# Kernel tuning notes

Hardware: AMD Instinct MI355X
Metric: run time of the kernel (lower is better)

## Reference

```python
import jax, jax.numpy as jnp
import numpy as np

INS, OUTS = 768, 64
B, S = 8, 2048


def setup_inputs() -> dict:
    key = jax.random.key(0)
    ks = jax.random.split(key, 7)
    scale = 1.0 / np.sqrt(INS)
    inputs = jax.random.normal(ks[0], (B, S, INS), dtype=jnp.float32)
    Wq = jax.random.uniform(ks[1], (INS, OUTS), jnp.float32, -scale, scale)
    bq = jax.random.uniform(ks[2], (OUTS,), jnp.float32, -scale, scale)
    Wk = jax.random.uniform(ks[3], (INS, OUTS), jnp.float32, -scale, scale)
    bk = jax.random.uniform(ks[4], (OUTS,), jnp.float32, -scale, scale)
    Wv = jax.random.uniform(ks[5], (INS, OUTS), jnp.float32, -scale, scale)
    bv = jax.random.uniform(ks[6], (OUTS,), jnp.float32, -scale, scale)
    return {"inputs": inputs, "Wq": Wq, "bq": bq, "Wk": Wk, "bk": bk, "Wv": Wv, "bv": bv}


def reference(inputs, Wq, bq, Wk, bk, Wv, bv):
    # QKV projections: [B, S, ins] @ [ins, outs] -> [B, S, outs]
    q = jnp.einsum('bsi,io->bso', inputs, Wq) + bq
    k = jnp.einsum('bsi,io->bso', inputs, Wk) + bk
    v = jnp.einsum('bsi,io->bso', inputs, Wv) + bv
    dim_k = k.shape[-1]
    # scores: [B, S, S] (materialized, as in the original bmm-based impl)
    att = jnp.einsum('bqd,bkd->bqk', q, k) / jnp.sqrt(jnp.asarray(dim_k, q.dtype))
    att_soft = jax.nn.softmax(att, axis=-1)
    out = jnp.einsum('bqk,bkd->bqd', att_soft, v)
    return out
```

## Files before the change

### kernel.cpp

```cpp
#include <hip/hip_runtime.h>
#include <hip/hip_bf16.h>
#include <stdint.h>

#define INS 768
#define OUTS 64
#define BB 8
#define SS 2048
#define LDP 40

typedef __attribute__((ext_vector_type(8))) short short8;
typedef __attribute__((ext_vector_type(4))) float f32x4;

__device__ inline unsigned short f2bf(float f) {
  union { float f; uint32_t u; } v; v.f = f;
  uint32_t r = v.u + 0x7FFFu + ((v.u >> 16) & 1u);
  return (unsigned short)(r >> 16);
}

__device__ inline short8 cvt8hw(float4 a, float4 b) {
  union { __hip_bfloat162 h[4]; short8 s; } u;
  u.h[0] = __float22bfloat162_rn(make_float2(a.x, a.y));
  u.h[1] = __float22bfloat162_rn(make_float2(a.z, a.w));
  u.h[2] = __float22bfloat162_rn(make_float2(b.x, b.y));
  u.h[3] = __float22bfloat162_rn(make_float2(b.z, b.w));
  return u.s;
}

__device__ inline void gl_lds16(const void* g, void* l) {
  __builtin_amdgcn_global_load_lds(
      (const __attribute__((address_space(1))) uint32_t*)g,
      (__attribute__((address_space(3))) uint32_t*)l, 16, 0, 0);
}

__device__ inline void memfence_sched() { asm volatile("" ::: "memory"); }

#define PIPE_BARRIER(N)                                        \
  do {                                                         \
    asm volatile("s_waitcnt vmcnt(" #N ")" ::: "memory");      \
    __builtin_amdgcn_s_barrier();                              \
    __builtin_amdgcn_sched_barrier(0);                         \
  } while (0)

__global__ __launch_bounds__(256) void prep(
    const float* __restrict__ Wq, const float* __restrict__ Wk,
    const float* __restrict__ Wv, unsigned short* __restrict__ WT) {
  const int idx = blockIdx.x * 256 + threadIdx.x;
  const int m = idx / (INS * OUTS);
  const int r = idx - m * (INS * OUTS);
  const int k = r >> 6, n = r & 63;
  const float* W = (m == 0) ? Wq : (m == 1) ? Wk : Wv;
  const float s = (m == 0) ? 0.125f : 1.0f;
  WT[((size_t)m * OUTS + n) * INS + k] = f2bf(W[(size_t)k * OUTS + n] * s);
}

__global__ __launch_bounds__(256) void qkv(
    const float* __restrict__ X, const unsigned short* __restrict__ WT,
    const float* __restrict__ bq, const float* __restrict__ bk,
    const float* __restrict__ bv,
    unsigned short* __restrict__ Qg, unsigned short* __restrict__ Kg,
    unsigned short* __restrict__ Vtg) {
  __shared__ __align__(16) float Xs[4][1024];
  const int tid  = threadIdx.x;
  const int wave = tid >> 6, lane = tid & 63;
  const int quad = lane >> 4, l16 = lane & 15;
  const int chg  = wave;
  const int row0 = blockIdx.x * 32;

  const int sr = tid >> 3, ss = tid & 7;
  const char* gsrc =
      (const char*)(X + (size_t)(row0 + sr) * INS) + ((ss ^ (sr & 7)) << 4);
  char* ldsb = (char*)&Xs[0][0] + wave * 1024;

  const float* Bm[3]; float scl[3]; int col0[3];
  const unsigned short* Wt[3];
#pragma unroll
  for (int nt = 0; nt < 3; ++nt) {
    const int n0 = chg * 48 + nt * 16;
    const int mat = n0 >> 6;
    col0[nt] = n0 & 63;
    Wt[nt] = WT + ((size_t)mat * OUTS + col0[nt] + l16) * INS + quad * 8;
    if (mat == 0)      { Bm[nt] = bq; scl[nt] = 0.125f; }
    else if (mat == 1) { Bm[nt] = bk; scl[nt] = 1.0f; }
    else               { Bm[nt] = bv; scl[nt] = 1.0f; }
  }

  int off0[2], off1[2];
#pragma unroll
  for (int fr = 0; fr < 2; ++fr) {
    const int lr = fr * 16 + l16;
    off0[fr] = lr * 128 + ((((quad << 1)    ) ^ (lr & 7)) << 4);
    off1[fr] = lr * 128 + ((((quad << 1) | 1) ^ (lr & 7)) << 4);
  }

  f32x4 acc[2][3];
#pragma unroll
  for (int fr = 0; fr < 2; ++fr)
#pragma unroll
    for (int nt = 0; nt < 3; ++nt) acc[fr][nt] = (f32x4){0.f, 0.f, 0.f, 0.f};

  short8 wb[3][3];

  gl_lds16(gsrc, ldsb);
#pragma unroll
  for (int nt = 0; nt < 3; ++nt)
    wb[0][nt] = *reinterpret_cast<const short8*>(Wt[nt]);
  memfence_sched();
  gl_lds16(gsrc + 128, ldsb + 4096);
  gl_lds16(gsrc + 256, ldsb + 8192);
#pragma unroll
  for (int nt = 0; nt < 3; ++nt)
    wb[1][nt] = *reinterpret_cast<const short8*>(Wt[nt] + 32);

#pragma unroll
  for (int kc = 0; kc < 24; ++kc) {
    if (kc <= 21)      PIPE_BARRIER(4);
    else if (kc == 22) PIPE_BARRIER(3);
    else               PIPE_BARRIER(0);

    const char* xb = (const char*)&Xs[kc & 3][0];
    float4 f00 = *reinterpret_cast<const float4*>(xb + off0[0]);
    float4 f01 = *reinterpret_cast<const float4*>(xb + off1[0]);
    float4 f10 = *reinterpret_cast<const float4*>(xb + off0[1]);
    float4 f11 = *reinterpret_cast<const float4*>(xb + off1[1]);
    short8 a0 = cvt8hw(f00, f01);
    short8 a1 = cvt8hw(f10, f11);
#pragma unroll
    for (int nt = 0; nt < 3; ++nt) {
      acc[0][nt] = __builtin_amdgcn_mfma_f32_16x16x32_bf16(a0, wb[kc % 3][nt], acc[0][nt], 0, 0, 0);
      acc[1][nt] = __builtin_amdgcn_mfma_f32_16x16x32_bf16(a1, wb[kc % 3][nt], acc[1][nt], 0, 0, 0);
    }
    if (kc + 3 < 24)
      gl_lds16(gsrc + (size_t)(kc + 3) * 128, ldsb + (size_t)((kc + 3) & 3) * 4096);
    if (kc + 2 < 24) {
#pragma unroll
      for (int nt = 0; nt < 3; ++nt)
        wb[(kc + 2) % 3][nt] =
            *reinterpret_cast<const short8*>(Wt[nt] + (kc + 2) * 32);
    }
  }

#pragma unroll
  for (int fr = 0; fr < 2; ++fr) {
    const int gm0 = row0 + fr * 16 + quad * 4;
#pragma unroll
    for (int nt = 0; nt < 3; ++nt) {
      const int n = chg * 48 + nt * 16 + l16;
      const float bias = Bm[nt][col0[nt] + l16] * scl[nt];
      if (n < 128) {
        unsigned short* dstbase = (n < 64) ? Qg : Kg;
        const int nn = n & 63;
#pragma unroll
        for (int r = 0; r < 4; ++r)
          dstbase[(size_t)(gm0 + r) * OUTS + nn] = f2bf(acc[fr][nt][r] + bias);
      } else {
        const int d = n - 128;
        const int batch = gm0 >> 11, s0 = gm0 & 2047;
        ushort4 pk;
        pk.x = f2bf(acc[fr][nt][0] + bias);
        pk.y = f2bf(acc[fr][nt][1] + bias);
        pk.z = f2bf(acc[fr][nt][2] + bias);
        pk.w = f2bf(acc[fr][nt][3] + bias);
        *reinterpret_cast<ushort4*>(&Vtg[((size_t)batch * OUTS + d) * SS + s0]) = pk;
      }
    }
  }
}

__global__ __launch_bounds__(256) void attn(
    const unsigned short* __restrict__ Qg, const unsigned short* __restrict__ Kg,
    const unsigned short* __restrict__ Vtg,
    float* __restrict__ OP, float* __restrict__ LS) {
  __shared__ __align__(16) char KsB[4][4096];
  __shared__ __align__(16) char VsB[4][4096];
  __shared__ __align__(16) unsigned short Ps[4][2][16 * LDP];
  const int tid  = threadIdx.x;
  const int wave = tid >> 6, lane = tid & 63;
  const int quad = lane >> 4, l16 = lane & 15;
  const int bt  = blockIdx.x >> 6;
  const int rem = blockIdx.x & 63;
  const int qb  = rem >> 2, ksl = rem & 3;
  const int q0 = qb * 128 + wave * 32;
  const unsigned short* Qb = Qg + (size_t)bt * SS * OUTS;
  const unsigned short* Kb = Kg + (size_t)bt * SS * OUTS;
  const unsigned short* Vb = Vtg + (size_t)bt * OUTS * SS;
  const int jbeg = ksl * 512;

  const int krow = wave * 8 + (lane >> 3), ks8 = lane & 7;
  const int vrow = wave * 16 + (lane >> 2), vs4 = lane & 3;
  const int vsw  = (vrow & 3) ^ ((vrow >> 2) & 3);
  const char* ksrc = (const char*)(Kb + (size_t)(jbeg + krow) * OUTS) +
                     ((ks8 ^ (krow & 7)) << 4);
  const char* vsrc = (const char*)(Vb + (size_t)vrow * SS + jbeg) +
                     ((vs4 ^ vsw) << 4);

  short8 aq[2][2];
#pragma unroll
  for (int mh = 0; mh < 2; ++mh)
#pragma unroll
    for (int ks = 0; ks < 2; ++ks)
      aq[mh][ks] = *reinterpret_cast<const short8*>(
          Qb + (size_t)(q0 + mh * 16 + l16) * OUTS + ks * 32 + quad * 8);

  int koff[2][2];
#pragma unroll
  for (int nt2 = 0; nt2 < 2; ++nt2)
#pragma unroll
    for (int ks = 0; ks < 2; ++ks)
      koff[nt2][ks] = (nt2 * 16 + l16) * 128 +
                      ((((ks << 2) | quad) ^ (l16 & 7)) << 4);
  int voff[4];
#pragma unroll
  for (int nt = 0; nt < 4; ++nt) {
    const int dr = nt * 16 + l16;
    voff[nt] = dr * 64 + ((quad ^ ((dr & 3) ^ ((dr >> 2) & 3))) << 4);
  }

  f32x4 oacc[2][4];
#pragma unroll
  for (int mh = 0; mh < 2; ++mh)
#pragma unroll
    for (int nt = 0; nt < 4; ++nt) oacc[mh][nt] = (f32x4){0.f, 0.f, 0.f, 0.f};
  float lsum[2][4] = {{0.f,0.f,0.f,0.f},{0.f,0.f,0.f,0.f}};

  memfence_sched();
  gl_lds16(ksrc,                      &KsB[0][0] + wave * 1024);
  gl_lds16(vsrc,                      &VsB[0][0] + wave * 1024);
  gl_lds16(ksrc + (size_t)1 * 4096,   &KsB[1][0] + wave * 1024);
  gl_lds16(vsrc + (size_t)1 * 64,     &VsB[1][0] + wave * 1024);
  gl_lds16(ksrc + (size_t)2 * 4096,   &KsB[2][0] + wave * 1024);
  gl_lds16(vsrc + (size_t)2 * 64,     &VsB[2][0] + wave * 1024);

#pragma unroll
  for (int kc = 0; kc < 16; ++kc) {
    if (kc <= 13)      PIPE_BARRIER(4);
    else if (kc == 14) PIPE_BARRIER(2);
    else               PIPE_BARRIER(0);

    const char* kb8 = &KsB[kc & 3][0];
    const char* vb8 = &VsB[kc & 3][0];
    short8 bk[2][2], bv[4];
#pragma unroll
    for (int nt2 = 0; nt2 < 2; ++nt2)
#pragma unroll
      for (int ks = 0; ks < 2; ++ks)
        bk[nt2][ks] = *reinterpret_cast<const short8*>(kb8 + koff[nt2][ks]);
#pragma unroll
    for (int nt = 0; nt < 4; ++nt)
      bv[nt] = *reinterpret_cast<const short8*>(vb8 + voff[nt]);

#pragma unroll
    for (int mh = 0; mh < 2; ++mh) {
      f32x4 sc[2];
      sc[0] = (f32x4){0.f,0.f,0.f,0.f}; sc[1] = (f32x4){0.f,0.f,0.f,0.f};
#pragma unroll
      for (int ks = 0; ks < 2; ++ks)
#pragma unroll
        for (int nt2 = 0; nt2 < 2; ++nt2)
          sc[nt2] = __builtin_amdgcn_mfma_f32_16x16x32_bf16(aq[mh][ks], bk[nt2][ks], sc[nt2], 0, 0, 0);

      unsigned short* Pw = Ps[wave][mh];
#pragma unroll
      for (int nt2 = 0; nt2 < 2; ++nt2)
#pragma unroll
        for (int r = 0; r < 4; ++r) {
          float p = __expf(sc[nt2][r]);
          lsum[mh][r] += p;
          Pw[(quad * 4 + r) * LDP + nt2 * 16 + l16] = f2bf(p);
        }
      short8 ap = *reinterpret_cast<const short8*>(&Pw[l16 * LDP + quad * 8]);
#pragma unroll
      for (int nt = 0; nt < 4; ++nt)
        oacc[mh][nt] = __builtin_amdgcn_mfma_f32_16x16x32_bf16(ap, bv[nt], oacc[mh][nt], 0, 0, 0);
    }

    if (kc + 3 < 16) {
      gl_lds16(ksrc + (size_t)(kc + 3) * 4096, &KsB[(kc + 3) & 3][0] + wave * 1024);
      gl_lds16(vsrc + (size_t)(kc + 3) * 64,   &VsB[(kc + 3) & 3][0] + wave * 1024);
    }
  }

#pragma unroll
  for (int st = 1; st < 16; st <<= 1)
#pragma unroll
    for (int mh = 0; mh < 2; ++mh)
#pragma unroll
      for (int r = 0; r < 4; ++r) lsum[mh][r] += __shfl_xor(lsum[mh][r], st, 64);

  float* OPb = OP + ((size_t)ksl * BB + bt) * SS * OUTS;
#pragma unroll
  for (int mh = 0; mh < 2; ++mh)
#pragma unroll
    for (int nt = 0; nt < 4; ++nt)
#pragma unroll
      for (int r = 0; r < 4; ++r) {
        int q = q0 + mh * 16 + quad * 4 + r;
        OPb[(size_t)q * OUTS + nt * 16 + l16] = oacc[mh][nt][r];
      }
  if (l16 == 0) {
#pragma unroll
    for (int mh = 0; mh < 2; ++mh)
#pragma unroll
      for (int r = 0; r < 4; ++r)
        LS[(size_t)ksl * BB * SS + bt * SS + q0 + mh * 16 + quad * 4 + r] = lsum[mh][r];
  }
}

__global__ __launch_bounds__(256) void combine(
    const float* __restrict__ OP, const float* __restrict__ LS,
    float* __restrict__ out) {
  const size_t i4 = (size_t)blockIdx.x * 256 + threadIdx.x;
  const size_t row = (i4 * 4) >> 6;
  float4 o = make_float4(0.f, 0.f, 0.f, 0.f);
  float l = 0.f;
#pragma unroll
  for (int ks = 0; ks < 4; ++ks) {
    float4 t = reinterpret_cast<const float4*>(OP + (size_t)ks * BB * SS * OUTS)[i4];
    o.x += t.x; o.y += t.y; o.z += t.z; o.w += t.w;
    l += LS[(size_t)ks * BB * SS + row];
  }
  const float inv = 1.0f / l;
  reinterpret_cast<float4*>(out)[i4] = make_float4(o.x * inv, o.y * inv, o.z * inv, o.w * inv);
}

extern "C" void kernel_launch(void* const* d_in, const int* in_sizes, int n_in,
                              void* d_out, int out_size, void* d_ws, size_t ws_size,
                              hipStream_t stream) {
  const float* X  = (const float*)d_in[0];
  const float* Wq = (const float*)d_in[1];
  const float* bq = (const float*)d_in[2];
  const float* Wk = (const float*)d_in[3];
  const float* bk = (const float*)d_in[4];
  const float* Wv = (const float*)d_in[5];
  const float* bv = (const float*)d_in[6];
  float* out = (float*)d_out;

  char* ws = (char*)d_ws;
  unsigned short* Qg  = (unsigned short*)(ws);
  unsigned short* Kg  = (unsigned short*)(ws + (size_t)2 * 1024 * 1024);
  unsigned short* Vtg = (unsigned short*)(ws + (size_t)4 * 1024 * 1024);
  unsigned short* WT  = (unsigned short*)(ws + (size_t)6 * 1024 * 1024);
  float*          OP  = (float*)(ws + (size_t)7 * 1024 * 1024);
  float*          LS  = (float*)(ws + (size_t)23 * 1024 * 1024);

  prep<<<576, 256, 0, stream>>>(Wq, Wk, Wv, WT);
  qkv<<<512, 256, 0, stream>>>(X, WT, bq, bk, bv, Qg, Kg, Vtg);
  attn<<<512, 256, 0, stream>>>(Qg, Kg, Vtg, OP, LS);
  combine<<<1024, 256, 0, stream>>>(OP, LS, out);
}
```

Measured before the change: 138.4 us.

## Fuse prep, qkv, attn and combine into one persistent cooperative kernel

Turns the four kernels into device functions and runs them in one persistent cooperative kernel of 256 blocks. Grid-wide syncs separate the stages, and each block loops over the 512 work units of qkv and attn. The aim is to remove the launch gaps and tail drains between kernels. In exchange each CU runs only one block at a time, which lowers occupancy and latency hiding. Shared memory is also reused across loop iterations without a trailing barrier, so the early prefetch of the next unit could race with reads from the previous one. The original multi-kernel path is kept as a fallback when the stream is being captured or the cooperative launch fails.

```diff
diff --git a/kernel.cpp b/kernel.cpp
--- a/kernel.cpp
+++ b/kernel.cpp
@@ -1,6 +1,9 @@
 #include <hip/hip_runtime.h>
 #include <hip/hip_bf16.h>
+#include <hip/hip_cooperative_groups.h>
 #include <stdint.h>
+
+namespace cg = cooperative_groups;
 
 #define INS 768
 #define OUTS 64
@@ -41,10 +44,10 @@
     __builtin_amdgcn_sched_barrier(0);                         \
   } while (0)
 
-__global__ __launch_bounds__(256) void prep(
-    const float* __restrict__ Wq, const float* __restrict__ Wk,
+
+__device__ __forceinline__ void prep_item(
+    int idx, const float* __restrict__ Wq, const float* __restrict__ Wk,
     const float* __restrict__ Wv, unsigned short* __restrict__ WT) {
-  const int idx = blockIdx.x * 256 + threadIdx.x;
   const int m = idx / (INS * OUTS);
   const int r = idx - m * (INS * OUTS);
   const int k = r >> 6, n = r & 63;
@@ -53,23 +56,22 @@
   WT[((size_t)m * OUTS + n) * INS + k] = f2bf(W[(size_t)k * OUTS + n] * s);
 }
 
-__global__ __launch_bounds__(256) void qkv(
-    const float* __restrict__ X, const unsigned short* __restrict__ WT,
+__device__ __forceinline__ void qkv_body(
+    int u, const float* __restrict__ X, const unsigned short* __restrict__ WT,
     const float* __restrict__ bq, const float* __restrict__ bk,
     const float* __restrict__ bv,
     unsigned short* __restrict__ Qg, unsigned short* __restrict__ Kg,
-    unsigned short* __restrict__ Vtg) {
-  __shared__ __align__(16) float Xs[4][1024];
+    unsigned short* __restrict__ Vtg, char* Xs ) {
   const int tid  = threadIdx.x;
   const int wave = tid >> 6, lane = tid & 63;
   const int quad = lane >> 4, l16 = lane & 15;
   const int chg  = wave;
-  const int row0 = blockIdx.x * 32;
+  const int row0 = u * 32;
 
   const int sr = tid >> 3, ss = tid & 7;
   const char* gsrc =
       (const char*)(X + (size_t)(row0 + sr) * INS) + ((ss ^ (sr & 7)) << 4);
-  char* ldsb = (char*)&Xs[0][0] + wave * 1024;
+  char* ldsb = Xs + wave * 1024;
 
   const float* Bm[3]; float scl[3]; int col0[3];
   const unsigned short* Wt[3];
@@ -117,7 +119,7 @@
     else if (kc == 22) PIPE_BARRIER(3);
     else               PIPE_BARRIER(0);
 
-    const char* xb = (const char*)&Xs[kc & 3][0];
+    const char* xb = Xs + (kc & 3) * 4096;
     float4 f00 = *reinterpret_cast<const float4*>(xb + off0[0]);
     float4 f01 = *reinterpret_cast<const float4*>(xb + off1[0]);
     float4 f10 = *reinterpret_cast<const float4*>(xb + off0[1]);
@@ -166,18 +168,16 @@
   }
 }
 
-__global__ __launch_bounds__(256) void attn(
-    const unsigned short* __restrict__ Qg, const unsigned short* __restrict__ Kg,
-    const unsigned short* __restrict__ Vtg,
-    float* __restrict__ OP, float* __restrict__ LS) {
-  __shared__ __align__(16) char KsB[4][4096];
-  __shared__ __align__(16) char VsB[4][4096];
-  __shared__ __align__(16) unsigned short Ps[4][2][16 * LDP];
+__device__ __forceinline__ void attn_body(
+    int u, const unsigned short* __restrict__ Qg,
+    const unsigned short* __restrict__ Kg, const unsigned short* __restrict__ Vtg,
+    float* __restrict__ OP, float* __restrict__ LS,
+    char* KsB , char* VsB , unsigned short* Ps ) {
   const int tid  = threadIdx.x;
   const int wave = tid >> 6, lane = tid & 63;
   const int quad = lane >> 4, l16 = lane & 15;
-  const int bt  = blockIdx.x >> 6;
-  const int rem = blockIdx.x & 63;
+  const int bt  = u >> 6;
+  const int rem = u & 63;
   const int qb  = rem >> 2, ksl = rem & 3;
   const int q0 = qb * 128 + wave * 32;
   const unsigned short* Qb = Qg + (size_t)bt * SS * OUTS;
@@ -223,12 +223,12 @@
   float lsum[2][4] = {{0.f,0.f,0.f,0.f},{0.f,0.f,0.f,0.f}};
 
   memfence_sched();
-  gl_lds16(ksrc,                      &KsB[0][0] + wave * 1024);
-  gl_lds16(vsrc,                      &VsB[0][0] + wave * 1024);
-  gl_lds16(ksrc + (size_t)1 * 4096,   &KsB[1][0] + wave * 1024);
-  gl_lds16(vsrc + (size_t)1 * 64,     &VsB[1][0] + wave * 1024);
-  gl_lds16(ksrc + (size_t)2 * 4096,   &KsB[2][0] + wave * 1024);
-  gl_lds16(vsrc + (size_t)2 * 64,     &VsB[2][0] + wave * 1024);
+  gl_lds16(ksrc,                    KsB + 0 * 4096 + wave * 1024);
+  gl_lds16(vsrc,                    VsB + 0 * 4096 + wave * 1024);
+  gl_lds16(ksrc + (size_t)1 * 4096, KsB + 1 * 4096 + wave * 1024);
+  gl_lds16(vsrc + (size_t)1 * 64,   VsB + 1 * 4096 + wave * 1024);
+  gl_lds16(ksrc + (size_t)2 * 4096, KsB + 2 * 4096 + wave * 1024);
+  gl_lds16(vsrc + (size_t)2 * 64,   VsB + 2 * 4096 + wave * 1024);
 
 #pragma unroll
   for (int kc = 0; kc < 16; ++kc) {
@@ -236,8 +236,8 @@
     else if (kc == 14) PIPE_BARRIER(2);
     else               PIPE_BARRIER(0);
 
-    const char* kb8 = &KsB[kc & 3][0];
-    const char* vb8 = &VsB[kc & 3][0];
+    const char* kb8 = KsB + (kc & 3) * 4096;
+    const char* vb8 = VsB + (kc & 3) * 4096;
     short8 bk[2][2], bv[4];
 #pragma unroll
     for (int nt2 = 0; nt2 < 2; ++nt2)
@@ -258,7 +258,7 @@
         for (int nt2 = 0; nt2 < 2; ++nt2)
           sc[nt2] = __builtin_amdgcn_mfma_f32_16x16x32_bf16(aq[mh][ks], bk[nt2][ks], sc[nt2], 0, 0, 0);
 
-      unsigned short* Pw = Ps[wave][mh];
+      unsigned short* Pw = Ps + (wave * 2 + mh) * (16 * LDP);
 #pragma unroll
       for (int nt2 = 0; nt2 < 2; ++nt2)
 #pragma unroll
@@ -274,8 +274,8 @@
     }
 
     if (kc + 3 < 16) {
-      gl_lds16(ksrc + (size_t)(kc + 3) * 4096, &KsB[(kc + 3) & 3][0] + wave * 1024);
-      gl_lds16(vsrc + (size_t)(kc + 3) * 64,   &VsB[(kc + 3) & 3][0] + wave * 1024);
+      gl_lds16(ksrc + (size_t)(kc + 3) * 4096, KsB + ((kc + 3) & 3) * 4096 + wave * 1024);
+      gl_lds16(vsrc + (size_t)(kc + 3) * 64,   VsB + ((kc + 3) & 3) * 4096 + wave * 1024);
     }
   }
 
@@ -305,10 +305,9 @@
   }
 }
 
-__global__ __launch_bounds__(256) void combine(
-    const float* __restrict__ OP, const float* __restrict__ LS,
+__device__ __forceinline__ void combine_item(
+    size_t i4, const float* __restrict__ OP, const float* __restrict__ LS,
     float* __restrict__ out) {
-  const size_t i4 = (size_t)blockIdx.x * 256 + threadIdx.x;
   const size_t row = (i4 * 4) >> 6;
   float4 o = make_float4(0.f, 0.f, 0.f, 0.f);
   float l = 0.f;
@@ -320,6 +319,74 @@
   }
   const float inv = 1.0f / l;
   reinterpret_cast<float4*>(out)[i4] = make_float4(o.x * inv, o.y * inv, o.z * inv, o.w * inv);
+}
+
+
+__global__ __launch_bounds__(256) void prep(
+    const float* __restrict__ Wq, const float* __restrict__ Wk,
+    const float* __restrict__ Wv, unsigned short* __restrict__ WT) {
+  prep_item(blockIdx.x * 256 + threadIdx.x, Wq, Wk, Wv, WT);
+}
+
+__global__ __launch_bounds__(256) void qkv(
+    const float* __restrict__ X, const unsigned short* __restrict__ WT,
+    const float* __restrict__ bq, const float* __restrict__ bk,
+    const float* __restrict__ bv,
+    unsigned short* __restrict__ Qg, unsigned short* __restrict__ Kg,
+    unsigned short* __restrict__ Vtg) {
+  __shared__ __align__(16) char Xs[16384];
+  qkv_body(blockIdx.x, X, WT, bq, bk, bv, Qg, Kg, Vtg, Xs);
+}
+
+__global__ __launch_bounds__(256) void attn(
+    const unsigned short* __restrict__ Qg, const unsigned short* __restrict__ Kg,
+    const unsigned short* __restrict__ Vtg,
+    float* __restrict__ OP, float* __restrict__ LS) {
+  __shared__ __align__(16) char KsB[16384];
+  __shared__ __align__(16) char VsB[16384];
+  __shared__ __align__(16) unsigned short Ps[4 * 2 * 16 * LDP];
+  attn_body(blockIdx.x, Qg, Kg, Vtg, OP, LS, KsB, VsB, Ps);
+}
+
+__global__ __launch_bounds__(256) void combine(
+    const float* __restrict__ OP, const float* __restrict__ LS,
+    float* __restrict__ out) {
+  combine_item((size_t)blockIdx.x * 256 + threadIdx.x, OP, LS, out);
+}
+
+__global__ __launch_bounds__(256) void fused(
+    const float* __restrict__ X,
+    const float* __restrict__ Wq, const float* __restrict__ bq,
+    const float* __restrict__ Wk, const float* __restrict__ bk,
+    const float* __restrict__ Wv, const float* __restrict__ bv,
+    unsigned short* __restrict__ WT,
+    unsigned short* __restrict__ Qg, unsigned short* __restrict__ Kg,
+    unsigned short* __restrict__ Vtg,
+    float* __restrict__ OP, float* __restrict__ LS,
+    float* __restrict__ out) {
+  cg::grid_group grid = cg::this_grid();
+  __shared__ __align__(16) char smem[43008];
+
+  for (int idx = blockIdx.x * 256 + threadIdx.x; idx < 3 * INS * OUTS;
+       idx += gridDim.x * 256)
+    prep_item(idx, Wq, Wk, Wv, WT);
+  __threadfence();
+  grid.sync();
+
+  for (int u = blockIdx.x; u < 512; u += gridDim.x)
+    qkv_body(u, X, WT, bq, bk, bv, Qg, Kg, Vtg, smem);
+  __threadfence();
+  grid.sync();
+
+  for (int u = blockIdx.x; u < 512; u += gridDim.x)
+    attn_body(u, Qg, Kg, Vtg, OP, LS, smem, smem + 16384,
+              (unsigned short*)(smem + 32768));
+  __threadfence();
+  grid.sync();
+
+  for (size_t i4 = (size_t)blockIdx.x * 256 + threadIdx.x;
+       i4 < (size_t)BB * SS * OUTS / 4; i4 += (size_t)gridDim.x * 256)
+    combine_item(i4, OP, LS, out);
 }
 
 extern "C" void kernel_launch(void* const* d_in, const int* in_sizes, int n_in,
@@ -342,6 +409,18 @@
   float*          OP  = (float*)(ws + (size_t)7 * 1024 * 1024);
   float*          LS  = (float*)(ws + (size_t)23 * 1024 * 1024);
 
+  hipStreamCaptureStatus cs = hipStreamCaptureStatusNone;
+  (void)hipStreamIsCapturing(stream, &cs);
+  if (cs == hipStreamCaptureStatusNone) {
+    void* args[] = {(void*)&X,  (void*)&Wq, (void*)&bq, (void*)&Wk, (void*)&bk,
+                    (void*)&Wv, (void*)&bv, (void*)&WT, (void*)&Qg, (void*)&Kg,
+                    (void*)&Vtg, (void*)&OP, (void*)&LS, (void*)&out};
+    hipError_t err = hipLaunchCooperativeKernel((const void*)fused, dim3(256),
+                                                dim3(256), args, 0, stream);
+    if (err == hipSuccess) return;
+    (void)hipGetLastError();
+  }
+
   prep<<<576, 256, 0, stream>>>(Wq, Wk, Wv, WT);
   qkv<<<512, 256, 0, stream>>>(X, WT, bq, bk, bv, Qg, Kg, Vtg);
   attn<<<512, 256, 0, stream>>>(Qg, Kg, Vtg, OP, LS);
```

After: 139.8 us. Within noise of the previous version (+1.0%).

## Fuse split-K combine into attention via in-block LDS reduction across waves

Applied to the files above, without the earlier changes.

The attention kernel is restructured so each block handles 32 query rows, with its four waves each covering a quarter of the key range. The partial outputs and softmax sums are then reduced through shared memory and written to the final output directly. This removes the separate combine kernel and the round trip of the fp32 partial output and sum buffers through global memory. V is stored in a tiled layout so each wave can load its B operands straight from global memory into registers, with double buffering, while K keeps a 3-stage per-wave LDS pipeline without block barriers. In exchange, each block now uses more LDS and has less query-level parallelism per block.

```diff
diff --git a/kernel.cpp b/kernel.cpp
--- a/kernel.cpp
+++ b/kernel.cpp
@@ -33,6 +33,13 @@
 }
 
 __device__ inline void memfence_sched() { asm volatile("" ::: "memory"); }
+
+#define PIPE_WAIT(N)                                           \
+  do {                                                         \
+    asm volatile("s_waitcnt vmcnt(" #N ")" ::: "memory");      \
+    __builtin_amdgcn_sched_barrier(0);                         \
+  } while (0)
+#define SFENCE() __builtin_amdgcn_sched_barrier(0)
 
 #define PIPE_BARRIER(N)                                        \
   do {                                                         \
@@ -59,7 +66,7 @@
     const float* __restrict__ bv,
     unsigned short* __restrict__ Qg, unsigned short* __restrict__ Kg,
     unsigned short* __restrict__ Vtg) {
-  __shared__ __align__(16) float Xs[4][1024];
+  __shared__ __align__(16) char Xs[4][4096];
   const int tid  = threadIdx.x;
   const int wave = tid >> 6, lane = tid & 63;
   const int quad = lane >> 4, l16 = lane & 15;
@@ -69,7 +76,7 @@
   const int sr = tid >> 3, ss = tid & 7;
   const char* gsrc =
       (const char*)(X + (size_t)(row0 + sr) * INS) + ((ss ^ (sr & 7)) << 4);
-  char* ldsb = (char*)&Xs[0][0] + wave * 1024;
+  char* ldsb = &Xs[0][0] + wave * 1024;
 
   const float* Bm[3]; float scl[3]; int col0[3];
   const unsigned short* Wt[3];
@@ -117,7 +124,7 @@
     else if (kc == 22) PIPE_BARRIER(3);
     else               PIPE_BARRIER(0);
 
-    const char* xb = (const char*)&Xs[kc & 3][0];
+    const char* xb = &Xs[0][0] + (kc & 3) * 4096;
     float4 f00 = *reinterpret_cast<const float4*>(xb + off0[0]);
     float4 f01 = *reinterpret_cast<const float4*>(xb + off1[0]);
     float4 f10 = *reinterpret_cast<const float4*>(xb + off0[1]);
@@ -160,38 +167,45 @@
         pk.y = f2bf(acc[fr][nt][1] + bias);
         pk.z = f2bf(acc[fr][nt][2] + bias);
         pk.w = f2bf(acc[fr][nt][3] + bias);
-        *reinterpret_cast<ushort4*>(&Vtg[((size_t)batch * OUTS + d) * SS + s0]) = pk;
+        *reinterpret_cast<ushort4*>(
+            &Vtg[(((size_t)batch * 64 + (s0 >> 5)) * 64 + d) * 32 + (s0 & 31)]) = pk;
       }
     }
   }
 }
 
-__global__ __launch_bounds__(256) void attn(
+__global__ __launch_bounds__(256) void attn2(
     const unsigned short* __restrict__ Qg, const unsigned short* __restrict__ Kg,
-    const unsigned short* __restrict__ Vtg,
-    float* __restrict__ OP, float* __restrict__ LS) {
-  __shared__ __align__(16) char KsB[4][4096];
-  __shared__ __align__(16) char VsB[4][4096];
-  __shared__ __align__(16) unsigned short Ps[4][2][16 * LDP];
+    const unsigned short* __restrict__ Vtg, float* __restrict__ out) {
+  __shared__ __align__(16) char smem[59392];
+  unsigned short* Ps = (unsigned short*)(smem + 49152);
+
   const int tid  = threadIdx.x;
   const int wave = tid >> 6, lane = tid & 63;
   const int quad = lane >> 4, l16 = lane & 15;
-  const int bt  = blockIdx.x >> 6;
-  const int rem = blockIdx.x & 63;
-  const int qb  = rem >> 2, ksl = rem & 3;
-  const int q0 = qb * 128 + wave * 32;
+  const int bt = blockIdx.x >> 6;
+  const int qt = blockIdx.x & 63;
+  const int q0 = qt * 32;
   const unsigned short* Qb = Qg + (size_t)bt * SS * OUTS;
   const unsigned short* Kb = Kg + (size_t)bt * SS * OUTS;
-  const unsigned short* Vb = Vtg + (size_t)bt * OUTS * SS;
-  const int jbeg = ksl * 512;
-
-  const int krow = wave * 8 + (lane >> 3), ks8 = lane & 7;
-  const int vrow = wave * 16 + (lane >> 2), vs4 = lane & 3;
-  const int vsw  = (vrow & 3) ^ ((vrow >> 2) & 3);
-  const char* ksrc = (const char*)(Kb + (size_t)(jbeg + krow) * OUTS) +
-                     ((ks8 ^ (krow & 7)) << 4);
-  const char* vsrc = (const char*)(Vb + (size_t)vrow * SS + jbeg) +
-                     ((vs4 ^ vsw) << 4);
+  const int jw = wave * 512;
+
+  const char* ksrc = (const char*)(Kb + (size_t)(jw + (lane >> 3)) * OUTS) +
+                     ((((lane & 7)) ^ ((lane >> 3) & 7)) << 4);
+  char* kbuf = smem + wave * 3 * 4096;
+
+#define KSTAGE(kc)                                                          \
+  do {                                                                      \
+    const char* s_ = ksrc + (size_t)(kc) * 32 * 128;                        \
+    char* d_ = kbuf + ((kc) % 3) * 4096;                                    \
+    gl_lds16(s_,              d_);                                          \
+    gl_lds16(s_ +  8 * 128,   d_ + 1024);                                   \
+    gl_lds16(s_ + 16 * 128,   d_ + 2048);                                   \
+    gl_lds16(s_ + 24 * 128,   d_ + 3072);                                   \
+  } while (0)
+
+  const unsigned short* Vbase =
+      Vtg + ((size_t)bt * 64 + wave * 16) * 64 * 32;
 
   short8 aq[2][2];
 #pragma unroll
@@ -208,12 +222,6 @@
     for (int ks = 0; ks < 2; ++ks)
       koff[nt2][ks] = (nt2 * 16 + l16) * 128 +
                       ((((ks << 2) | quad) ^ (l16 & 7)) << 4);
-  int voff[4];
-#pragma unroll
-  for (int nt = 0; nt < 4; ++nt) {
-    const int dr = nt * 16 + l16;
-    voff[nt] = dr * 64 + ((quad ^ ((dr & 3) ^ ((dr >> 2) & 3))) << 4);
-  }
 
   f32x4 oacc[2][4];
 #pragma unroll
@@ -222,31 +230,37 @@
     for (int nt = 0; nt < 4; ++nt) oacc[mh][nt] = (f32x4){0.f, 0.f, 0.f, 0.f};
   float lsum[2][4] = {{0.f,0.f,0.f,0.f},{0.f,0.f,0.f,0.f}};
 
-  memfence_sched();
-  gl_lds16(ksrc,                      &KsB[0][0] + wave * 1024);
-  gl_lds16(vsrc,                      &VsB[0][0] + wave * 1024);
-  gl_lds16(ksrc + (size_t)1 * 4096,   &KsB[1][0] + wave * 1024);
-  gl_lds16(vsrc + (size_t)1 * 64,     &VsB[1][0] + wave * 1024);
-  gl_lds16(ksrc + (size_t)2 * 4096,   &KsB[2][0] + wave * 1024);
-  gl_lds16(vsrc + (size_t)2 * 64,     &VsB[2][0] + wave * 1024);
+  short8 bv[2][4];
+
+  KSTAGE(0);
+  SFENCE();
+#pragma unroll
+  for (int nt = 0; nt < 4; ++nt)
+    bv[0][nt] = *reinterpret_cast<const short8*>(
+        Vbase + (nt * 16 + l16) * 32 + quad * 8);
+  SFENCE();
+  KSTAGE(1);
+  SFENCE();
 
 #pragma unroll
   for (int kc = 0; kc < 16; ++kc) {
-    if (kc <= 13)      PIPE_BARRIER(4);
-    else if (kc == 14) PIPE_BARRIER(2);
-    else               PIPE_BARRIER(0);
-
-    const char* kb8 = &KsB[kc & 3][0];
-    const char* vb8 = &VsB[kc & 3][0];
-    short8 bk[2][2], bv[4];
+    if (kc < 15) PIPE_WAIT(8); else PIPE_WAIT(4);
+
+    if (kc + 1 < 16) {
+#pragma unroll
+      for (int nt = 0; nt < 4; ++nt)
+        bv[(kc + 1) & 1][nt] = *reinterpret_cast<const short8*>(
+            Vbase + (size_t)(kc + 1) * 2048 + (nt * 16 + l16) * 32 + quad * 8);
+      SFENCE();
+    }
+
+    const char* kb8 = kbuf + (kc % 3) * 4096;
+    short8 bk[2][2];
 #pragma unroll
     for (int nt2 = 0; nt2 < 2; ++nt2)
 #pragma unroll
       for (int ks = 0; ks < 2; ++ks)
         bk[nt2][ks] = *reinterpret_cast<const short8*>(kb8 + koff[nt2][ks]);
-#pragma unroll
-    for (int nt = 0; nt < 4; ++nt)
-      bv[nt] = *reinterpret_cast<const short8*>(vb8 + voff[nt]);
 
 #pragma unroll
     for (int mh = 0; mh < 2; ++mh) {
@@ -258,7 +272,7 @@
         for (int nt2 = 0; nt2 < 2; ++nt2)
           sc[nt2] = __builtin_amdgcn_mfma_f32_16x16x32_bf16(aq[mh][ks], bk[nt2][ks], sc[nt2], 0, 0, 0);
 
-      unsigned short* Pw = Ps[wave][mh];
+      unsigned short* Pw = Ps + (wave * 2 + mh) * (16 * LDP);
 #pragma unroll
       for (int nt2 = 0; nt2 < 2; ++nt2)
 #pragma unroll
@@ -270,12 +284,13 @@
       short8 ap = *reinterpret_cast<const short8*>(&Pw[l16 * LDP + quad * 8]);
 #pragma unroll
       for (int nt = 0; nt < 4; ++nt)
-        oacc[mh][nt] = __builtin_amdgcn_mfma_f32_16x16x32_bf16(ap, bv[nt], oacc[mh][nt], 0, 0, 0);
-    }
-
-    if (kc + 3 < 16) {
-      gl_lds16(ksrc + (size_t)(kc + 3) * 4096, &KsB[(kc + 3) & 3][0] + wave * 1024);
-      gl_lds16(vsrc + (size_t)(kc + 3) * 64,   &VsB[(kc + 3) & 3][0] + wave * 1024);
+        oacc[mh][nt] = __builtin_amdgcn_mfma_f32_16x16x32_bf16(ap, bv[kc & 1][nt], oacc[mh][nt], 0, 0, 0);
+    }
+
+    if (kc + 2 < 16) {
+      SFENCE();
+      KSTAGE(kc + 2);
+      SFENCE();
     }
   }
 
@@ -286,40 +301,40 @@
 #pragma unroll
       for (int r = 0; r < 4; ++r) lsum[mh][r] += __shfl_xor(lsum[mh][r], st, 64);
 
-  float* OPb = OP + ((size_t)ksl * BB + bt) * SS * OUTS;
-#pragma unroll
-  for (int mh = 0; mh < 2; ++mh)
+  __syncthreads();
+  float* Cmb = (float*)smem;
+  const int cb = (wave * 64 + lane) * 41;
+#pragma unroll
+  for (int mh = 0; mh < 2; ++mh) {
 #pragma unroll
     for (int nt = 0; nt < 4; ++nt)
 #pragma unroll
-      for (int r = 0; r < 4; ++r) {
-        int q = q0 + mh * 16 + quad * 4 + r;
-        OPb[(size_t)q * OUTS + nt * 16 + l16] = oacc[mh][nt][r];
+      for (int r = 0; r < 4; ++r)
+        Cmb[cb + (mh * 4 + nt) * 4 + r] = oacc[mh][nt][r];
+#pragma unroll
+    for (int r = 0; r < 4; ++r) Cmb[cb + 32 + mh * 4 + r] = lsum[mh][r];
+  }
+  __syncthreads();
+
+  float* outb = out + ((size_t)bt * SS + q0) * OUTS;
+#pragma unroll
+  for (int i = 0; i < 2; ++i) {
+    const int p = wave * 2 + i;
+    const int mh = p >> 2, nt = p & 3;
+#pragma unroll
+    for (int r = 0; r < 4; ++r) {
+      float o = 0.f, l = 0.f;
+#pragma unroll
+      for (int w = 0; w < 4; ++w) {
+        o += Cmb[(w * 64 + lane) * 41 + (mh * 4 + nt) * 4 + r];
+        l += Cmb[(w * 64 + lane) * 41 + 32 + mh * 4 + r];
       }
-  if (l16 == 0) {
-#pragma unroll
-    for (int mh = 0; mh < 2; ++mh)
-#pragma unroll
-      for (int r = 0; r < 4; ++r)
-        LS[(size_t)ksl * BB * SS + bt * SS + q0 + mh * 16 + quad * 4 + r] = lsum[mh][r];
-  }
-}
-
-__global__ __launch_bounds__(256) void combine(
-    const float* __restrict__ OP, const float* __restrict__ LS,
-    float* __restrict__ out) {
-  const size_t i4 = (size_t)blockIdx.x * 256 + threadIdx.x;
-  const size_t row = (i4 * 4) >> 6;
-  float4 o = make_float4(0.f, 0.f, 0.f, 0.f);
-  float l = 0.f;
-#pragma unroll
-  for (int ks = 0; ks < 4; ++ks) {
-    float4 t = reinterpret_cast<const float4*>(OP + (size_t)ks * BB * SS * OUTS)[i4];
-    o.x += t.x; o.y += t.y; o.z += t.z; o.w += t.w;
-    l += LS[(size_t)ks * BB * SS + row];
-  }
-  const float inv = 1.0f / l;
-  reinterpret_cast<float4*>(out)[i4] = make_float4(o.x * inv, o.y * inv, o.z * inv, o.w * inv);
+      const float inv = 1.0f / l;
+      const int q = mh * 16 + quad * 4 + r;
+      outb[(size_t)q * OUTS + nt * 16 + l16] = o * inv;
+    }
+  }
+#undef KSTAGE
 }
 
 extern "C" void kernel_launch(void* const* d_in, const int* in_sizes, int n_in,
@@ -339,11 +354,8 @@
   unsigned short* Kg  = (unsigned short*)(ws + (size_t)2 * 1024 * 1024);
   unsigned short* Vtg = (unsigned short*)(ws + (size_t)4 * 1024 * 1024);
   unsigned short* WT  = (unsigned short*)(ws + (size_t)6 * 1024 * 1024);
-  float*          OP  = (float*)(ws + (size_t)7 * 1024 * 1024);
-  float*          LS  = (float*)(ws + (size_t)23 * 1024 * 1024);
 
   prep<<<576, 256, 0, stream>>>(Wq, Wk, Wv, WT);
   qkv<<<512, 256, 0, stream>>>(X, WT, bq, bk, bv, Qg, Kg, Vtg);
-  attn<<<512, 256, 0, stream>>>(Qg, Kg, Vtg, OP, LS);
-  combine<<<1024, 256, 0, stream>>>(OP, LS, out);
-}
+  attn2<<<512, 256, 0, stream>>>(Qg, Kg, Vtg, out);
+}
```

Result: no change. 140.5 us (+1.6%).

## Widen attention key tiles to 64 and switch to double-buffered staging

Applied to the files above, without the earlier changes.

The attention kernel now processes 64 keys per iteration over 8 iterations instead of 32 keys over 16. K/V shared-memory tiles are double-buffered, replacing the 4-deep ring, and use a new 128-byte-row XOR swizzle. Each iteration issues twice as many score and PV MFMAs per barrier, which halves the number of block-wide barriers. In exchange, only one stage of prefetch hides global-load latency, and register and LDS use per iteration grow.

```diff
diff --git a/kernel.cpp b/kernel.cpp
--- a/kernel.cpp
+++ b/kernel.cpp
@@ -6,7 +6,7 @@
 #define OUTS 64
 #define BB 8
 #define SS 2048
-#define LDP 40
+#define LDP2 72
 
 typedef __attribute__((ext_vector_type(8))) short short8;
 typedef __attribute__((ext_vector_type(4))) float f32x4;
@@ -117,7 +117,7 @@
     else if (kc == 22) PIPE_BARRIER(3);
     else               PIPE_BARRIER(0);
 
-    const char* xb = (const char*)&Xs[kc & 3][0];
+    const char* xb = (const char*)&Xs[0][0] + (kc & 3) * 4096;
     float4 f00 = *reinterpret_cast<const float4*>(xb + off0[0]);
     float4 f01 = *reinterpret_cast<const float4*>(xb + off1[0]);
     float4 f10 = *reinterpret_cast<const float4*>(xb + off0[1]);
@@ -170,9 +170,9 @@
     const unsigned short* __restrict__ Qg, const unsigned short* __restrict__ Kg,
     const unsigned short* __restrict__ Vtg,
     float* __restrict__ OP, float* __restrict__ LS) {
-  __shared__ __align__(16) char KsB[4][4096];
-  __shared__ __align__(16) char VsB[4][4096];
-  __shared__ __align__(16) unsigned short Ps[4][2][16 * LDP];
+  __shared__ __align__(16) char KsB[2][8192];
+  __shared__ __align__(16) char VsB[2][8192];
+  __shared__ __align__(16) unsigned short Ps[4][2][16 * LDP2];
   const int tid  = threadIdx.x;
   const int wave = tid >> 6, lane = tid & 63;
   const int quad = lane >> 4, l16 = lane & 15;
@@ -185,13 +185,21 @@
   const unsigned short* Vb = Vtg + (size_t)bt * OUTS * SS;
   const int jbeg = ksl * 512;
 
-  const int krow = wave * 8 + (lane >> 3), ks8 = lane & 7;
-  const int vrow = wave * 16 + (lane >> 2), vs4 = lane & 3;
-  const int vsw  = (vrow & 3) ^ ((vrow >> 2) & 3);
-  const char* ksrc = (const char*)(Kb + (size_t)(jbeg + krow) * OUTS) +
-                     ((ks8 ^ (krow & 7)) << 4);
-  const char* vsrc = (const char*)(Vb + (size_t)vrow * SS + jbeg) +
-                     ((vs4 ^ vsw) << 4);
+  const int srow = lane >> 3, sslot = lane & 7;
+  const char* ksrc = (const char*)(Kb + (size_t)(jbeg + wave * 16 + srow) * OUTS) +
+                     ((sslot ^ srow) << 4);
+  const char* vsrc = (const char*)(Vb + (size_t)(wave * 16 + srow) * SS + jbeg) +
+                     ((sslot ^ srow) << 4);
+
+#define STAGE(kc)                                                            \
+  do {                                                                       \
+    char* kd = &KsB[(kc) & 1][0] + wave * 2048;                              \
+    char* vd = &VsB[(kc) & 1][0] + wave * 2048;                              \
+    gl_lds16(ksrc + (size_t)(kc) * 8192,          kd);                       \
+    gl_lds16(ksrc + (size_t)(kc) * 8192 + 1024,   kd + 1024);                \
+    gl_lds16(vsrc + (size_t)(kc) * 128,           vd);                       \
+    gl_lds16(vsrc + (size_t)(kc) * 128 + 8 * SS * 2, vd + 1024);             \
+  } while (0)
 
   short8 aq[2][2];
 #pragma unroll
@@ -201,19 +209,20 @@
       aq[mh][ks] = *reinterpret_cast<const short8*>(
           Qb + (size_t)(q0 + mh * 16 + l16) * OUTS + ks * 32 + quad * 8);
 
-  int koff[2][2];
-#pragma unroll
-  for (int nt2 = 0; nt2 < 2; ++nt2)
+  int koff[4][2];
+#pragma unroll
+  for (int nt2 = 0; nt2 < 4; ++nt2)
 #pragma unroll
     for (int ks = 0; ks < 2; ++ks)
       koff[nt2][ks] = (nt2 * 16 + l16) * 128 +
                       ((((ks << 2) | quad) ^ (l16 & 7)) << 4);
-  int voff[4];
-#pragma unroll
-  for (int nt = 0; nt < 4; ++nt) {
-    const int dr = nt * 16 + l16;
-    voff[nt] = dr * 64 + ((quad ^ ((dr & 3) ^ ((dr >> 2) & 3))) << 4);
-  }
+  int voff[2][4];
+#pragma unroll
+  for (int ks = 0; ks < 2; ++ks)
+#pragma unroll
+    for (int nt = 0; nt < 4; ++nt)
+      voff[ks][nt] = (nt * 16 + l16) * 128 +
+                     ((((ks << 2) | quad) ^ (l16 & 7)) << 4);
 
   f32x4 oacc[2][4];
 #pragma unroll
@@ -223,61 +232,58 @@
   float lsum[2][4] = {{0.f,0.f,0.f,0.f},{0.f,0.f,0.f,0.f}};
 
   memfence_sched();
-  gl_lds16(ksrc,                      &KsB[0][0] + wave * 1024);
-  gl_lds16(vsrc,                      &VsB[0][0] + wave * 1024);
-  gl_lds16(ksrc + (size_t)1 * 4096,   &KsB[1][0] + wave * 1024);
-  gl_lds16(vsrc + (size_t)1 * 64,     &VsB[1][0] + wave * 1024);
-  gl_lds16(ksrc + (size_t)2 * 4096,   &KsB[2][0] + wave * 1024);
-  gl_lds16(vsrc + (size_t)2 * 64,     &VsB[2][0] + wave * 1024);
-
-#pragma unroll
-  for (int kc = 0; kc < 16; ++kc) {
-    if (kc <= 13)      PIPE_BARRIER(4);
-    else if (kc == 14) PIPE_BARRIER(2);
-    else               PIPE_BARRIER(0);
-
-    const char* kb8 = &KsB[kc & 3][0];
-    const char* vb8 = &VsB[kc & 3][0];
-    short8 bk[2][2], bv[4];
-#pragma unroll
-    for (int nt2 = 0; nt2 < 2; ++nt2)
+  STAGE(0);
+
+#pragma unroll
+  for (int kc = 0; kc < 8; ++kc) {
+    PIPE_BARRIER(0);
+    if (kc + 1 < 8) STAGE(kc + 1);
+
+    const char* kb8 = &KsB[kc & 1][0];
+    const char* vb8 = &VsB[kc & 1][0];
+    short8 bk[4][2], bv[2][4];
+#pragma unroll
+    for (int nt2 = 0; nt2 < 4; ++nt2)
 #pragma unroll
       for (int ks = 0; ks < 2; ++ks)
         bk[nt2][ks] = *reinterpret_cast<const short8*>(kb8 + koff[nt2][ks]);
 #pragma unroll
-    for (int nt = 0; nt < 4; ++nt)
-      bv[nt] = *reinterpret_cast<const short8*>(vb8 + voff[nt]);
+    for (int ks = 0; ks < 2; ++ks)
+#pragma unroll
+      for (int nt = 0; nt < 4; ++nt)
+        bv[ks][nt] = *reinterpret_cast<const short8*>(vb8 + voff[ks][nt]);
 
 #pragma unroll
     for (int mh = 0; mh < 2; ++mh) {
-      f32x4 sc[2];
-      sc[0] = (f32x4){0.f,0.f,0.f,0.f}; sc[1] = (f32x4){0.f,0.f,0.f,0.f};
+      f32x4 sc[4];
+#pragma unroll
+      for (int nt2 = 0; nt2 < 4; ++nt2) sc[nt2] = (f32x4){0.f,0.f,0.f,0.f};
 #pragma unroll
       for (int ks = 0; ks < 2; ++ks)
 #pragma unroll
-        for (int nt2 = 0; nt2 < 2; ++nt2)
+        for (int nt2 = 0; nt2 < 4; ++nt2)
           sc[nt2] = __builtin_amdgcn_mfma_f32_16x16x32_bf16(aq[mh][ks], bk[nt2][ks], sc[nt2], 0, 0, 0);
 
-      unsigned short* Pw = Ps[wave][mh];
-#pragma unroll
-      for (int nt2 = 0; nt2 < 2; ++nt2)
+      unsigned short* Pw = &Ps[wave][mh][0];
+#pragma unroll
+      for (int nt2 = 0; nt2 < 4; ++nt2)
 #pragma unroll
         for (int r = 0; r < 4; ++r) {
           float p = __expf(sc[nt2][r]);
           lsum[mh][r] += p;
-          Pw[(quad * 4 + r) * LDP + nt2 * 16 + l16] = f2bf(p);
+          Pw[(quad * 4 + r) * LDP2 + nt2 * 16 + l16] = f2bf(p);
         }
-      short8 ap = *reinterpret_cast<const short8*>(&Pw[l16 * LDP + quad * 8]);
+      short8 ap0 = *reinterpret_cast<const short8*>(&Pw[l16 * LDP2 + quad * 8]);
+      short8 ap1 = *reinterpret_cast<const short8*>(&Pw[l16 * LDP2 + 32 + quad * 8]);
 #pragma unroll
       for (int nt = 0; nt < 4; ++nt)
-        oacc[mh][nt] = __builtin_amdgcn_mfma_f32_16x16x32_bf16(ap, bv[nt], oacc[mh][nt], 0, 0, 0);
+        oacc[mh][nt] = __builtin_amdgcn_mfma_f32_16x16x32_bf16(ap0, bv[0][nt], oacc[mh][nt], 0, 0, 0);
+#pragma unroll
+      for (int nt = 0; nt < 4; ++nt)
+        oacc[mh][nt] = __builtin_amdgcn_mfma_f32_16x16x32_bf16(ap1, bv[1][nt], oacc[mh][nt], 0, 0, 0);
     }
-
-    if (kc + 3 < 16) {
-      gl_lds16(ksrc + (size_t)(kc + 3) * 4096, &KsB[(kc + 3) & 3][0] + wave * 1024);
-      gl_lds16(vsrc + (size_t)(kc + 3) * 64,   &VsB[(kc + 3) & 3][0] + wave * 1024);
-    }
-  }
+  }
+#undef STAGE
 
 #pragma unroll
   for (int st = 1; st < 16; st <<= 1)
```

Result: no change. 139.6 us (+0.9%).
